# Performance work log

Measured on AMD Instinct MI355X. Metric: run time of the kernel, lower is better.

## Reference

```python
import jax, jax.numpy as jnp
import numpy as np

B, C, H, W = 16, 10, 400, 352
N = 50  # objects per sample
ZSIZE = 1.0 - (-3.0)  # maxZ - minZ
MEANDIMS = jnp.array([1.52, 1.63, 3.88], dtype=jnp.float32)
BKG_THRESH = 0.025
LOG_CLAMP = -100.0  # torch BCE clamps log at -100


def setup_inputs() -> dict:
    key = jax.random.key(0)
    k1, k2, k3, k4, k5, k6 = jax.random.split(key, 6)
    output = jax.random.normal(k1, (B, C, H, W), dtype=jnp.float32)
    # target columns: x, y, z, h, w, l, angle
    x = jax.random.uniform(k2, (B, N), minval=0.0, maxval=H / 2 - 1e-3)
    y = jax.random.uniform(k3, (B, N), minval=0.0, maxval=W / 2 - 1e-3)
    z = jax.random.uniform(k4, (B, N), minval=0.0, maxval=ZSIZE)
    dims = jax.random.uniform(k5, (B, N, 3), minval=0.5, maxval=5.0)
    ang = jax.random.uniform(k6, (B, N), minval=-np.pi, maxval=np.pi)
    target = jnp.concatenate(
        [x[..., None], y[..., None], z[..., None], dims, ang[..., None]], axis=-1
    ).astype(jnp.float32)
    return {"output": output, "target": target}


def _per_sample(out_i, tgt_i):
    # out_i: [H, W, C], tgt_i: [N, 7]
    tx = tgt_i[:, 0] * 2.0
    ty = tgt_i[:, 1] * 2.0
    dx = jnp.floor(tx).astype(jnp.int32)
    dy = jnp.floor(ty).astype(jnp.int32)

    # background mask: True everywhere except object cells
    bkgmask = jnp.ones((H, W), dtype=bool).at[dx, dy].set(False)
    out0 = out_i[:, :, 0]
    bkg_p = jax.nn.sigmoid(out0)
    nbkg = bkgmask.sum()
    clsscale = jnp.exp(-3.0 * (bkg_p * bkgmask).sum() / nbkg) * 2.5

    # BCE(bkg, 0) over background cells with p > 0.025 (skip if none)
    sel = bkgmask & (bkg_p > BKG_THRESH)
    cnt = sel.sum()
    logv = jnp.maximum(jax.nn.log_sigmoid(-out0), LOG_CLAMP)  # log(1-sigmoid)
    bkg_l = jnp.where(
        cnt > 0,
        -(jnp.where(sel, logv, 0.0)).sum() / jnp.maximum(cnt, 1).astype(jnp.float32),
        0.0,
    )

    # gather per-object predictions: [N, C]
    out_g = out_i[dx, dy, :]

    fx = tx - jnp.floor(tx)
    fy = ty - jnp.floor(ty)
    tz = tgt_i[:, 2] / ZSIZE
    hwl_t = jnp.log(tgt_i[:, 3:6] / MEANDIMS)
    angle = tgt_i[:, 6]
    anglecls = (angle >= 0).astype(jnp.int32)

    # BCE(sigmoid(out[:,0]), 1) * clsscale
    objcls_l = (-jnp.maximum(jax.nn.log_sigmoid(out_g[:, 0]), LOG_CLAMP)).mean() * clsscale

    # MSE(sigmoid(out[:,1:4]), [fx,fy,tz])
    xyz_t = jnp.stack([fx, fy, tz], axis=1)
    xyz_l = ((jax.nn.sigmoid(out_g[:, 1:4]) - xyz_t) ** 2).mean()

    # MSE(out[:,4:7], log(dims/meandims)) * 0.5
    hwl_l = ((out_g[:, 4:7] - hwl_t) ** 2).mean() * 0.5

    # CE(out[:,7:9], anglecls) * 0.5
    ls = jax.nn.log_softmax(out_g[:, 7:9], axis=1)
    anglecls_l = (-jnp.take_along_axis(ls, anglecls[:, None], axis=1)).mean() * 0.5

    # smooth_l1(sin(out[:,9]), sin(sin(angle))) * 0.5   (tgt[:,8]=sin(angle), then .sin() again)
    d = jnp.sin(out_g[:, 9]) - jnp.sin(jnp.sin(angle))
    ad = jnp.abs(d)
    anglesin_l = jnp.where(ad < 1.0, 0.5 * d * d, ad - 0.5).mean() * 0.5

    return jnp.stack([bkg_l, objcls_l, xyz_l, hwl_l, anglecls_l, anglesin_l])


def _compute(output, target):
    out = jnp.transpose(output, (0, 2, 3, 1))  # [B, H, W, C]
    terms = jax.vmap(_per_sample)(out, target)  # [B, 6]
    sums = terms.sum(axis=0)
    total = sums.sum()
    return total, sums


def reference(output, target):
    total, s = _compute(output, target)
    return (total, s[0], s[1], s[2], s[3], s[4], s[5])
```

## Files before the change

### kernel.cpp

```cpp
#include <hip/hip_runtime.h>
#include <math.h>

#define Bn 16
#define Cn 10
#define Hn 400
#define Wn 352
#define Nn 50
#define PLANE (Hn * Wn)
#define NCHUNK 32
#define VPER (PLANE / 4 / NCHUNK)
#define BKG_THRESH 0.025f
#define LOG_CLAMP -100.0f

#define WS_PV 2048

__device__ __forceinline__ float softplusf(float x) {
    return fmaxf(x, 0.0f) + log1pf(expf(-fabsf(x)));
}
__device__ __forceinline__ float sigmoidf(float x) {
    return 1.0f / (1.0f + expf(-x));
}
__device__ __forceinline__ float wave_sum(float v) {
    for (int off = 32; off > 0; off >>= 1) v += __shfl_down(v, off);
    return __shfl(v, 0);
}

__global__ __launch_bounds__(256) void partial_kernel(const float* __restrict__ out,
                                                      const float* __restrict__ tgt,
                                                      float* __restrict__ ws) {
    const int tid = threadIdx.x;

    if (blockIdx.x < Bn * NCHUNK) {
        const int b  = blockIdx.x >> 5;
        const int ch = blockIdx.x & 31;
        const float4* plane = (const float4*)(out + (size_t)b * Cn * PLANE);
        const int i0 = ch * VPER + tid;

        float4 v0 = plane[i0];
        float4 v1 = plane[i0 + 256];
        float4 v2 = plane[i0 + 512];
        float4 v3 = plane[i0 + 768];

        float s_sig = 0.0f, s_log = 0.0f, s_cnt = 0.0f;
        float xs[16];
        xs[0]=v0.x; xs[1]=v0.y; xs[2]=v0.z; xs[3]=v0.w;
        xs[4]=v1.x; xs[5]=v1.y; xs[6]=v1.z; xs[7]=v1.w;
        xs[8]=v2.x; xs[9]=v2.y; xs[10]=v2.z; xs[11]=v2.w;
        xs[12]=v3.x; xs[13]=v3.y; xs[14]=v3.z; xs[15]=v3.w;
        #pragma unroll
        for (int k = 0; k < 16; ++k) {
            float x = xs[k];
            float p = sigmoidf(x);
            s_sig += p;
            bool sel = p > BKG_THRESH;
            s_cnt += sel ? 1.0f : 0.0f;
            s_log += sel ? fmaxf(-softplusf(x), LOG_CLAMP) : 0.0f;
        }
        if (tid < VPER - 1024) {
            float4 v4 = plane[i0 + 1024];
            float ys[4] = {v4.x, v4.y, v4.z, v4.w};
            #pragma unroll
            for (int k = 0; k < 4; ++k) {
                float x = ys[k];
                float p = sigmoidf(x);
                s_sig += p;
                bool sel = p > BKG_THRESH;
                s_cnt += sel ? 1.0f : 0.0f;
                s_log += sel ? fmaxf(-softplusf(x), LOG_CLAMP) : 0.0f;
            }
        }

        s_sig = wave_sum(s_sig);
        s_log = wave_sum(s_log);
        s_cnt = wave_sum(s_cnt);

        __shared__ float sh[4][3];
        const int wv = tid >> 6, lane6 = tid & 63;
        if (lane6 == 0) { sh[wv][0] = s_sig; sh[wv][1] = s_log; sh[wv][2] = s_cnt; }
        __syncthreads();
        if (tid == 0) {
            float* p = ws + (size_t)(b * NCHUNK + ch) * 3;
            p[0] = sh[0][0] + sh[1][0] + sh[2][0] + sh[3][0];
            p[1] = sh[0][1] + sh[1][1] + sh[2][1] + sh[3][1];
            p[2] = sh[0][2] + sh[1][2] + sh[2][2] + sh[3][2];
        }
        return;
    }

    if (tid >= 64) return;
    const int b    = blockIdx.x - Bn * NCHUNK;
    const int lane = tid;

    const float* t = tgt + (size_t)b * Nn * 7;
    const bool active = lane < Nn;
    float tx = 0.0f, ty = 0.0f, t2 = 0.0f, t3 = 1.0f, t4 = 1.0f, t5 = 1.0f, ang = 0.0f;
    int key = -1;
    if (active) {
        tx = t[lane * 7 + 0] * 2.0f;
        ty = t[lane * 7 + 1] * 2.0f;
        t2 = t[lane * 7 + 2];
        t3 = t[lane * 7 + 3];
        t4 = t[lane * 7 + 4];
        t5 = t[lane * 7 + 5];
        ang = t[lane * 7 + 6];
        int dx = (int)floorf(tx);
        int dy = (int)floorf(ty);
        key = dx * Wn + dy;
    }

    bool isfirst = active;
    #pragma unroll 1
    for (int m = 0; m < Nn; ++m) {
        int km = __shfl(key, m);
        if (active && m < lane && km == key) isfirst = false;
    }

    const float* base = out + (size_t)b * Cn * PLANE;
    float g[10];
    #pragma unroll
    for (int c = 0; c < 10; ++c) g[c] = active ? base[(size_t)c * PLANE + key] : 0.0f;

    float c_sig = 0.0f, c_log = 0.0f, c_cnt = 0.0f, c_n = 0.0f;
    if (isfirst) {
        float p = sigmoidf(g[0]);
        c_sig = p;
        c_n = 1.0f;
        if (p > BKG_THRESH) {
            c_cnt = 1.0f;
            c_log = fmaxf(-softplusf(g[0]), LOG_CLAMP);
        }
    }

    float v_obj = 0.0f, v_xyz = 0.0f, v_hwl = 0.0f, v_acl = 0.0f, v_asin = 0.0f;
    if (active) {
        v_obj = -fmaxf(-softplusf(-g[0]), LOG_CLAMP);

        float fx = tx - floorf(tx);
        float fy = ty - floorf(ty);
        float tz = t2 * 0.25f;
        float e0 = sigmoidf(g[1]) - fx;
        float e1 = sigmoidf(g[2]) - fy;
        float e2 = sigmoidf(g[3]) - tz;
        v_xyz = e0 * e0 + e1 * e1 + e2 * e2;

        float h0 = g[4] - logf(t3 / 1.52f);
        float h1 = g[5] - logf(t4 / 1.63f);
        float h2 = g[6] - logf(t5 / 3.88f);
        v_hwl = h0 * h0 + h1 * h1 + h2 * h2;

        float m = fmaxf(g[7], g[8]);
        float lse = m + logf(expf(g[7] - m) + expf(g[8] - m));
        float gsel = (ang >= 0.0f) ? g[8] : g[7];
        v_acl = lse - gsel;

        float d = sinf(g[9]) - sinf(sinf(ang));
        float ad = fabsf(d);
        v_asin = (ad < 1.0f) ? 0.5f * d * d : ad - 0.5f;
    }
    v_obj  = wave_sum(v_obj);
    v_xyz  = wave_sum(v_xyz);
    v_hwl  = wave_sum(v_hwl);
    v_acl  = wave_sum(v_acl);
    v_asin = wave_sum(v_asin);
    c_sig  = wave_sum(c_sig);
    c_log  = wave_sum(c_log);
    c_cnt  = wave_sum(c_cnt);
    c_n    = wave_sum(c_n);

    if (lane == 0) {
        float* pv = ws + WS_PV + (size_t)b * 10;
        pv[0] = v_obj;  pv[1] = v_xyz; pv[2] = v_hwl; pv[3] = v_acl; pv[4] = v_asin;
        pv[5] = c_sig;  pv[6] = c_log; pv[7] = c_cnt; pv[8] = c_n;
    }
}

__global__ __launch_bounds__(1024) void finalize_kernel(const float* __restrict__ ws,
                                                        float* __restrict__ out7) {
    const int b    = threadIdx.x >> 6;
    const int lane = threadIdx.x & 63;

    float s_sig = 0.0f, s_log = 0.0f, s_cnt = 0.0f;
    if (lane < NCHUNK) {
        const float* p = ws + (size_t)(b * NCHUNK + lane) * 3;
        s_sig = p[0]; s_log = p[1]; s_cnt = p[2];
    }
    s_sig = wave_sum(s_sig);
    s_log = wave_sum(s_log);
    s_cnt = wave_sum(s_cnt);

    __shared__ float sh_terms[Bn][6];
    if (lane == 0) {
        const float* pv = ws + WS_PV + (size_t)b * 10;
        float v_obj = pv[0], v_xyz = pv[1], v_hwl = pv[2], v_acl = pv[3], v_asin = pv[4];
        float c_sig = pv[5], c_log = pv[6], c_cnt = pv[7], c_n = pv[8];

        float nbkg    = (float)PLANE - c_n;
        float sig_bkg = s_sig - c_sig;
        float clsscale = expf(-3.0f * sig_bkg / nbkg) * 2.5f;

        float cnt  = s_cnt - c_cnt;
        float slog = s_log - c_log;
        float bkg_l = (cnt > 0.0f) ? (-slog / fmaxf(cnt, 1.0f)) : 0.0f;

        const float invN  = 1.0f / (float)Nn;
        const float invN3 = 1.0f / (float)(Nn * 3);

        sh_terms[b][0] = bkg_l;
        sh_terms[b][1] = v_obj * invN * clsscale;
        sh_terms[b][2] = v_xyz * invN3;
        sh_terms[b][3] = v_hwl * invN3 * 0.5f;
        sh_terms[b][4] = v_acl * invN * 0.5f;
        sh_terms[b][5] = v_asin * invN * 0.5f;
    }
    __syncthreads();

    if (threadIdx.x == 0) {
        float s[6] = {0, 0, 0, 0, 0, 0};
        for (int bb = 0; bb < Bn; ++bb)
            for (int j = 0; j < 6; ++j)
                s[j] += sh_terms[bb][j];
        float tot = 0.0f;
        for (int j = 0; j < 6; ++j) tot += s[j];
        out7[0] = tot;
        for (int j = 0; j < 6; ++j) out7[1 + j] = s[j];
    }
}

extern "C" void kernel_launch(void* const* d_in, const int* in_sizes, int n_in,
                              void* d_out, int out_size, void* d_ws, size_t ws_size,
                              hipStream_t stream) {
    const float* out = (const float*)d_in[0];
    const float* tgt = (const float*)d_in[1];
    float* o  = (float*)d_out;
    float* ws = (float*)d_ws;

    partial_kernel<<<Bn * NCHUNK + Bn, 256, 0, stream>>>(out, tgt, ws);
    finalize_kernel<<<1, 1024, 0, stream>>>(ws, o);
}
```

Measured before the change: 21.08 us.

## Reorder gather blocks first, share exp between sigmoid and softplus, SoA workspace

Moves the per-sample object-gather blocks to the low block indices so they are scheduled first instead of trailing the plane-reduction blocks. The background pass now computes exp(-|x|) once and derives both the sigmoid and the softplus from it, replacing two exps and a division per element. The workspace partial sums change from interleaved triples to separate arrays, so the finalize kernel reads them with coalesced loads. The new sigmoid form is algebraically equivalent, but its rounding differs slightly from the old one.

```diff
diff --git a/kernel.cpp b/kernel.cpp
--- a/kernel.cpp
+++ b/kernel.cpp
@@ -12,7 +12,10 @@
 #define BKG_THRESH 0.025f
 #define LOG_CLAMP -100.0f
 
-#define WS_PV 2048
+#define WS_SIG 0
+#define WS_LOG 512
+#define WS_CNT 1024
+#define WS_PV  2048
 
 __device__ __forceinline__ float softplusf(float x) {
     return fmaxf(x, 0.0f) + log1pf(expf(-fabsf(x)));
@@ -30,147 +33,154 @@
                                                       float* __restrict__ ws) {
     const int tid = threadIdx.x;
 
-    if (blockIdx.x < Bn * NCHUNK) {
-        const int b  = blockIdx.x >> 5;
-        const int ch = blockIdx.x & 31;
-        const float4* plane = (const float4*)(out + (size_t)b * Cn * PLANE);
-        const int i0 = ch * VPER + tid;
-
-        float4 v0 = plane[i0];
-        float4 v1 = plane[i0 + 256];
-        float4 v2 = plane[i0 + 512];
-        float4 v3 = plane[i0 + 768];
-
-        float s_sig = 0.0f, s_log = 0.0f, s_cnt = 0.0f;
-        float xs[16];
-        xs[0]=v0.x; xs[1]=v0.y; xs[2]=v0.z; xs[3]=v0.w;
-        xs[4]=v1.x; xs[5]=v1.y; xs[6]=v1.z; xs[7]=v1.w;
-        xs[8]=v2.x; xs[9]=v2.y; xs[10]=v2.z; xs[11]=v2.w;
-        xs[12]=v3.x; xs[13]=v3.y; xs[14]=v3.z; xs[15]=v3.w;
+    if (blockIdx.x < Bn) {
+        if (tid >= 64) return;
+        const int b    = blockIdx.x;
+        const int lane = tid;
+
+        const float* t = tgt + (size_t)b * Nn * 7;
+        const bool active = lane < Nn;
+        float tx = 0.0f, ty = 0.0f, t2 = 0.0f, t3 = 1.0f, t4 = 1.0f, t5 = 1.0f, ang = 0.0f;
+        int key = -1;
+        if (active) {
+            tx = t[lane * 7 + 0] * 2.0f;
+            ty = t[lane * 7 + 1] * 2.0f;
+            t2 = t[lane * 7 + 2];
+            t3 = t[lane * 7 + 3];
+            t4 = t[lane * 7 + 4];
+            t5 = t[lane * 7 + 5];
+            ang = t[lane * 7 + 6];
+            int dx = (int)floorf(tx);
+            int dy = (int)floorf(ty);
+            key = dx * Wn + dy;
+        }
+
+        bool isfirst = active;
+        #pragma unroll 1
+        for (int m = 0; m < Nn; ++m) {
+            int km = __shfl(key, m);
+            if (active && m < lane && km == key) isfirst = false;
+        }
+
+        const float* base = out + (size_t)b * Cn * PLANE;
+        float g[10];
         #pragma unroll
-        for (int k = 0; k < 16; ++k) {
-            float x = xs[k];
-            float p = sigmoidf(x);
+        for (int c = 0; c < 10; ++c) g[c] = active ? base[(size_t)c * PLANE + key] : 0.0f;
+
+        float c_sig = 0.0f, c_log = 0.0f, c_cnt = 0.0f, c_n = 0.0f;
+        if (isfirst) {
+            float p = sigmoidf(g[0]);
+            c_sig = p;
+            c_n = 1.0f;
+            if (p > BKG_THRESH) {
+                c_cnt = 1.0f;
+                c_log = fmaxf(-softplusf(g[0]), LOG_CLAMP);
+            }
+        }
+
+        float v_obj = 0.0f, v_xyz = 0.0f, v_hwl = 0.0f, v_acl = 0.0f, v_asin = 0.0f;
+        if (active) {
+            v_obj = -fmaxf(-softplusf(-g[0]), LOG_CLAMP);
+
+            float fx = tx - floorf(tx);
+            float fy = ty - floorf(ty);
+            float tz = t2 * 0.25f;
+            float e0 = sigmoidf(g[1]) - fx;
+            float e1 = sigmoidf(g[2]) - fy;
+            float e2 = sigmoidf(g[3]) - tz;
+            v_xyz = e0 * e0 + e1 * e1 + e2 * e2;
+
+            float h0 = g[4] - logf(t3 / 1.52f);
+            float h1 = g[5] - logf(t4 / 1.63f);
+            float h2 = g[6] - logf(t5 / 3.88f);
+            v_hwl = h0 * h0 + h1 * h1 + h2 * h2;
+
+            float m = fmaxf(g[7], g[8]);
+            float lse = m + logf(expf(g[7] - m) + expf(g[8] - m));
+            float gsel = (ang >= 0.0f) ? g[8] : g[7];
+            v_acl = lse - gsel;
+
+            float d = sinf(g[9]) - sinf(sinf(ang));
+            float ad = fabsf(d);
+            v_asin = (ad < 1.0f) ? 0.5f * d * d : ad - 0.5f;
+        }
+        v_obj  = wave_sum(v_obj);
+        v_xyz  = wave_sum(v_xyz);
+        v_hwl  = wave_sum(v_hwl);
+        v_acl  = wave_sum(v_acl);
+        v_asin = wave_sum(v_asin);
+        c_sig  = wave_sum(c_sig);
+        c_log  = wave_sum(c_log);
+        c_cnt  = wave_sum(c_cnt);
+        c_n    = wave_sum(c_n);
+
+        if (lane == 0) {
+            float* pv = ws + WS_PV + (size_t)b * 10;
+            pv[0] = v_obj;  pv[1] = v_xyz; pv[2] = v_hwl; pv[3] = v_acl; pv[4] = v_asin;
+            pv[5] = c_sig;  pv[6] = c_log; pv[7] = c_cnt; pv[8] = c_n;
+        }
+        return;
+    }
+
+    const int idx = blockIdx.x - Bn;
+    const int b  = idx >> 5;
+    const int ch = idx & 31;
+    const float4* plane = (const float4*)(out + (size_t)b * Cn * PLANE);
+    const int i0 = ch * VPER + tid;
+
+    float4 v0 = plane[i0];
+    float4 v1 = plane[i0 + 256];
+    float4 v2 = plane[i0 + 512];
+    float4 v3 = plane[i0 + 768];
+
+    float s_sig = 0.0f, s_log = 0.0f, s_cnt = 0.0f;
+    float xs[16];
+    xs[0]=v0.x; xs[1]=v0.y; xs[2]=v0.z; xs[3]=v0.w;
+    xs[4]=v1.x; xs[5]=v1.y; xs[6]=v1.z; xs[7]=v1.w;
+    xs[8]=v2.x; xs[9]=v2.y; xs[10]=v2.z; xs[11]=v2.w;
+    xs[12]=v3.x; xs[13]=v3.y; xs[14]=v3.z; xs[15]=v3.w;
+    #pragma unroll
+    for (int k = 0; k < 16; ++k) {
+        float x = xs[k];
+        float e   = expf(-fabsf(x));
+        float inv = 1.0f / (1.0f + e);
+        float p   = (x >= 0.0f) ? inv : e * inv;
+        float sp  = fmaxf(x, 0.0f) + log1pf(e);
+        s_sig += p;
+        bool sel = p > BKG_THRESH;
+        s_cnt += sel ? 1.0f : 0.0f;
+        s_log += sel ? fmaxf(-sp, LOG_CLAMP) : 0.0f;
+    }
+    if (tid < VPER - 1024) {
+        float4 v4 = plane[i0 + 1024];
+        float ys[4] = {v4.x, v4.y, v4.z, v4.w};
+        #pragma unroll
+        for (int k = 0; k < 4; ++k) {
+            float x = ys[k];
+            float e   = expf(-fabsf(x));
+            float inv = 1.0f / (1.0f + e);
+            float p   = (x >= 0.0f) ? inv : e * inv;
+            float sp  = fmaxf(x, 0.0f) + log1pf(e);
             s_sig += p;
             bool sel = p > BKG_THRESH;
             s_cnt += sel ? 1.0f : 0.0f;
-            s_log += sel ? fmaxf(-softplusf(x), LOG_CLAMP) : 0.0f;
-        }
-        if (tid < VPER - 1024) {
-            float4 v4 = plane[i0 + 1024];
-            float ys[4] = {v4.x, v4.y, v4.z, v4.w};
-            #pragma unroll
-            for (int k = 0; k < 4; ++k) {
-                float x = ys[k];
-                float p = sigmoidf(x);
-                s_sig += p;
-                bool sel = p > BKG_THRESH;
-                s_cnt += sel ? 1.0f : 0.0f;
-                s_log += sel ? fmaxf(-softplusf(x), LOG_CLAMP) : 0.0f;
-            }
-        }
-
-        s_sig = wave_sum(s_sig);
-        s_log = wave_sum(s_log);
-        s_cnt = wave_sum(s_cnt);
-
-        __shared__ float sh[4][3];
-        const int wv = tid >> 6, lane6 = tid & 63;
-        if (lane6 == 0) { sh[wv][0] = s_sig; sh[wv][1] = s_log; sh[wv][2] = s_cnt; }
-        __syncthreads();
-        if (tid == 0) {
-            float* p = ws + (size_t)(b * NCHUNK + ch) * 3;
-            p[0] = sh[0][0] + sh[1][0] + sh[2][0] + sh[3][0];
-            p[1] = sh[0][1] + sh[1][1] + sh[2][1] + sh[3][1];
-            p[2] = sh[0][2] + sh[1][2] + sh[2][2] + sh[3][2];
-        }
-        return;
-    }
-
-    if (tid >= 64) return;
-    const int b    = blockIdx.x - Bn * NCHUNK;
-    const int lane = tid;
-
-    const float* t = tgt + (size_t)b * Nn * 7;
-    const bool active = lane < Nn;
-    float tx = 0.0f, ty = 0.0f, t2 = 0.0f, t3 = 1.0f, t4 = 1.0f, t5 = 1.0f, ang = 0.0f;
-    int key = -1;
-    if (active) {
-        tx = t[lane * 7 + 0] * 2.0f;
-        ty = t[lane * 7 + 1] * 2.0f;
-        t2 = t[lane * 7 + 2];
-        t3 = t[lane * 7 + 3];
-        t4 = t[lane * 7 + 4];
-        t5 = t[lane * 7 + 5];
-        ang = t[lane * 7 + 6];
-        int dx = (int)floorf(tx);
-        int dy = (int)floorf(ty);
-        key = dx * Wn + dy;
-    }
-
-    bool isfirst = active;
-    #pragma unroll 1
-    for (int m = 0; m < Nn; ++m) {
-        int km = __shfl(key, m);
-        if (active && m < lane && km == key) isfirst = false;
-    }
-
-    const float* base = out + (size_t)b * Cn * PLANE;
-    float g[10];
-    #pragma unroll
-    for (int c = 0; c < 10; ++c) g[c] = active ? base[(size_t)c * PLANE + key] : 0.0f;
-
-    float c_sig = 0.0f, c_log = 0.0f, c_cnt = 0.0f, c_n = 0.0f;
-    if (isfirst) {
-        float p = sigmoidf(g[0]);
-        c_sig = p;
-        c_n = 1.0f;
-        if (p > BKG_THRESH) {
-            c_cnt = 1.0f;
-            c_log = fmaxf(-softplusf(g[0]), LOG_CLAMP);
-        }
-    }
-
-    float v_obj = 0.0f, v_xyz = 0.0f, v_hwl = 0.0f, v_acl = 0.0f, v_asin = 0.0f;
-    if (active) {
-        v_obj = -fmaxf(-softplusf(-g[0]), LOG_CLAMP);
-
-        float fx = tx - floorf(tx);
-        float fy = ty - floorf(ty);
-        float tz = t2 * 0.25f;
-        float e0 = sigmoidf(g[1]) - fx;
-        float e1 = sigmoidf(g[2]) - fy;
-        float e2 = sigmoidf(g[3]) - tz;
-        v_xyz = e0 * e0 + e1 * e1 + e2 * e2;
-
-        float h0 = g[4] - logf(t3 / 1.52f);
-        float h1 = g[5] - logf(t4 / 1.63f);
-        float h2 = g[6] - logf(t5 / 3.88f);
-        v_hwl = h0 * h0 + h1 * h1 + h2 * h2;
-
-        float m = fmaxf(g[7], g[8]);
-        float lse = m + logf(expf(g[7] - m) + expf(g[8] - m));
-        float gsel = (ang >= 0.0f) ? g[8] : g[7];
-        v_acl = lse - gsel;
-
-        float d = sinf(g[9]) - sinf(sinf(ang));
-        float ad = fabsf(d);
-        v_asin = (ad < 1.0f) ? 0.5f * d * d : ad - 0.5f;
-    }
-    v_obj  = wave_sum(v_obj);
-    v_xyz  = wave_sum(v_xyz);
-    v_hwl  = wave_sum(v_hwl);
-    v_acl  = wave_sum(v_acl);
-    v_asin = wave_sum(v_asin);
-    c_sig  = wave_sum(c_sig);
-    c_log  = wave_sum(c_log);
-    c_cnt  = wave_sum(c_cnt);
-    c_n    = wave_sum(c_n);
-
-    if (lane == 0) {
-        float* pv = ws + WS_PV + (size_t)b * 10;
-        pv[0] = v_obj;  pv[1] = v_xyz; pv[2] = v_hwl; pv[3] = v_acl; pv[4] = v_asin;
-        pv[5] = c_sig;  pv[6] = c_log; pv[7] = c_cnt; pv[8] = c_n;
+            s_log += sel ? fmaxf(-sp, LOG_CLAMP) : 0.0f;
+        }
+    }
+
+    s_sig = wave_sum(s_sig);
+    s_log = wave_sum(s_log);
+    s_cnt = wave_sum(s_cnt);
+
+    __shared__ float sh[4][3];
+    const int wv = tid >> 6, lane6 = tid & 63;
+    if (lane6 == 0) { sh[wv][0] = s_sig; sh[wv][1] = s_log; sh[wv][2] = s_cnt; }
+    __syncthreads();
+    if (tid == 0) {
+        const int slot = b * NCHUNK + ch;
+        ws[WS_SIG + slot] = sh[0][0] + sh[1][0] + sh[2][0] + sh[3][0];
+        ws[WS_LOG + slot] = sh[0][1] + sh[1][1] + sh[2][1] + sh[3][1];
+        ws[WS_CNT + slot] = sh[0][2] + sh[1][2] + sh[2][2] + sh[3][2];
     }
 }
 
@@ -181,8 +191,10 @@
 
     float s_sig = 0.0f, s_log = 0.0f, s_cnt = 0.0f;
     if (lane < NCHUNK) {
-        const float* p = ws + (size_t)(b * NCHUNK + lane) * 3;
-        s_sig = p[0]; s_log = p[1]; s_cnt = p[2];
+        const int slot = b * NCHUNK + lane;
+        s_sig = ws[WS_SIG + slot];
+        s_log = ws[WS_LOG + slot];
+        s_cnt = ws[WS_CNT + slot];
     }
     s_sig = wave_sum(s_sig);
     s_log = wave_sum(s_log);
```

Result: faster. 19.64 us (median of 2 runs) (-6.8%).
